# Optimization experiments

Hardware: AMD Instinct MI355X
Metric: run time of the kernel (lower is better)

## Reference

```python
import jax, jax.numpy as jnp
import numpy as np

NL = 192
SCALE = 1.5
SH_C0 = 0.28209479177387814
SH_C1 = 0.4886025119029199
SH_C2 = [1.0925484305920792, -1.0925484305920792, 0.31539156525252005, -1.0925484305920792, 0.5462742152960396]


def sh_eval(k, d):
    # k: (N, 3, 9) SH coeffs, d: (N, 3) directions -> (N, 3) rgb
    x, y, z = d[..., 0:1], d[..., 1:2], d[..., 2:3]
    return (SH_C0 * k[..., 0]
            - SH_C1 * y * k[..., 1]
            + SH_C1 * z * k[..., 2]
            - SH_C1 * x * k[..., 3]
            + SH_C2[0] * x * y * k[..., 4]
            + SH_C2[1] * y * z * k[..., 5]
            + SH_C2[2] * (2.0 * z * z - x * x - y * y) * k[..., 6]
            + SH_C2[3] * x * z * k[..., 7]
            + SH_C2[4] * (x * x - y * y) * k[..., 8])


def setup_inputs() -> dict:
    key = jax.random.key(0)
    k1, k2 = jax.random.split(key)
    N = 1048576
    x = jax.random.normal(k1, (N, 3), dtype=jnp.float32)
    d = jax.random.normal(k2, (N, 3), dtype=jnp.float32)
    voxel = jnp.ones((NL, NL, NL, 28), dtype=jnp.float32) / 100.0
    return {"x": x, "d": d, "voxel": voxel}


def reference(x, d, voxel):
    xs = x / SCALE
    mask = jnp.all(jnp.abs(xs) < 0.5, axis=1)  # (N,)
    # continuous grid coordinates, clipped like the original
    idx = jnp.clip(xs / (2.0 / NL) + NL / 2.0, 0.0, NL - 1.0)  # (N,3)
    xf = jnp.floor(idx)
    xc = jnp.ceil(idx)
    f = xf.astype(jnp.int32)
    c = xc.astype(jnp.int32)
    # 8 vertices in the ORIGINAL module's ordering (incl. its patch-layout quirk)
    vx = jnp.stack([f[:, 0], c[:, 0], f[:, 0], f[:, 0], f[:, 0], c[:, 0], c[:, 0], c[:, 0]], axis=1)
    vy = jnp.stack([f[:, 1], f[:, 1], c[:, 1], f[:, 1], c[:, 1], f[:, 1], c[:, 1], c[:, 1]], axis=1)
    vz = jnp.stack([f[:, 2], f[:, 2], f[:, 2], c[:, 2], c[:, 2], c[:, 2], f[:, 2], c[:, 2]], axis=1)
    v = voxel[vx, vy, vz]  # (N, 8, 28) gather
    # grid_sample trilinear weights on the 2x2x2 patch: slot j=(dd,hh,ww),
    # w-frac = t0, h-frac = t1, d-frac = t2 (align_corners=False, size 2 => frac = t)
    t = idx - xf  # (N,3)
    t0, t1, t2 = t[:, 0], t[:, 1], t[:, 2]
    u0, u1, u2 = 1.0 - t0, 1.0 - t1, 1.0 - t2
    w = jnp.stack([u2 * u1 * u0, u2 * u1 * t0, u2 * t1 * u0, u2 * t1 * t0,
                   t2 * u1 * u0, t2 * u1 * t0, t2 * t1 * u0, t2 * t1 * t0], axis=1)  # (N,8)
    feat = jnp.einsum('nk,nkc->nc', w, v)  # (N,28)
    sigma = jnp.where(mask, jax.nn.relu(feat[:, 0]), 0.0)  # (N,)
    k = feat[:, 1:].reshape(-1, 3, 9)
    color = jnp.where(mask[:, None], sh_eval(k, d), 0.0)  # (N,3)
    return color, sigma
```

## Files before the change

### kernel.cpp

```cpp
#include <hip/hip_runtime.h>


#define VNL 192

#define SH_C0f 0.28209479177387814f
#define SH_C1f 0.4886025119029199f
#define C2_0f  1.0925484305920792f
#define C2_1f (-1.0925484305920792f)
#define C2_2f  0.31539156525252005f
#define C2_3f (-1.0925484305920792f)
#define C2_4f  0.5462742152960396f

__global__ __launch_bounds__(256) void plen_fused_kernel(
    const float* __restrict__ x,
    const float* __restrict__ d,
    const float* __restrict__ voxel,
    float* __restrict__ out,
    int N)
{
    int i = blockIdx.x * 256 + threadIdx.x;
    const int lane = threadIdx.x & 63;
    const int g = lane >> 3;
    const int j = lane & 7;

    bool act = false;
    float px = 0.f, py = 0.f, pz = 0.f;
    float vdx = 0.f, vdy = 0.f, vdz = 0.f;
    if (i < N) {
        px = x[3 * i + 0] / 1.5f;
        py = x[3 * i + 1] / 1.5f;
        pz = x[3 * i + 2] / 1.5f;
        act = (fabsf(px) < 0.5f) && (fabsf(py) < 0.5f) && (fabsf(pz) < 0.5f);
        vdx = d[3 * i + 0];
        vdy = d[3 * i + 1];
        vdz = d[3 * i + 2];
        if (!act) {
            out[3 * i + 0] = 0.f;
            out[3 * i + 1] = 0.f;
            out[3 * i + 2] = 0.f;
            out[(size_t)3 * N + i] = 0.f;
        }
    }

    unsigned long long bal = __ballot(act);
    int nact = (int)__popcll(bal);

    for (int c = 0; c * 8 < nact; ++c) {
        int r = c * 8 + g;
        bool gact = (r < nact);
        int rr = gact ? r : 0;

        unsigned long long m = bal;
        for (int k = 0; k < rr; ++k) m &= (m - 1);
        int owner = (int)__builtin_ctzll(m);

        float ppx = __shfl(px,  owner);
        float ppy = __shfl(py,  owner);
        float ppz = __shfl(pz,  owner);
        float pdx = __shfl(vdx, owner);
        float pdy = __shfl(vdy, owner);
        float pdz = __shfl(vdz, owner);
        int   pi  = __shfl(i,   owner);

        if (gact) {
            const float step = 2.0f / (float)VNL;
            float ix = fminf(fmaxf(ppx / step + (float)(VNL / 2), 0.0f), (float)(VNL - 1));
            float iy = fminf(fmaxf(ppy / step + (float)(VNL / 2), 0.0f), (float)(VNL - 1));
            float iz = fminf(fmaxf(ppz / step + (float)(VNL / 2), 0.0f), (float)(VNL - 1));

            float fx = floorf(ix), fy = floorf(iy), fz = floorf(iz);
            int f0 = (int)fx, f1 = (int)fy, f2 = (int)fz;
            int c0i = (int)ceilf(ix), c1i = (int)ceilf(iy), c2i = (int)ceilf(iz);

            float t0 = ix - fx, t1 = iy - fy, t2 = iz - fz;
            float u0 = 1.0f - t0, u1 = 1.0f - t1, u2 = 1.0f - t2;

            float wj = ((j & 4) ? t2 : u2) * ((j & 2) ? t1 : u1) * ((j & 1) ? t0 : u0);

            int X = ((0xE2 >> j) & 1) ? c0i : f0;
            int Y = ((0xD4 >> j) & 1) ? c1i : f1;
            int Z = ((0xB8 >> j) & 1) ? c2i : f2;
            int off = ((X * VNL + Y) * VNL + Z) * 112;

            const char* cell = (const char*)voxel + (size_t)(unsigned)off;
            float4 v0 = *(const float4*)(cell +  0);
            float4 v1 = *(const float4*)(cell + 16);
            float4 v2 = *(const float4*)(cell + 32);
            float4 v3 = *(const float4*)(cell + 48);
            float4 v4 = *(const float4*)(cell + 64);
            float4 v5 = *(const float4*)(cell + 80);
            float4 v6 = *(const float4*)(cell + 96);

            float b1 = -SH_C1f * pdy;
            float b2 =  SH_C1f * pdz;
            float b3 = -SH_C1f * pdx;
            float b4 = C2_0f * pdx * pdy;
            float b5 = C2_1f * pdy * pdz;
            float b6 = C2_2f * (2.0f * pdz * pdz - pdx * pdx - pdy * pdy);
            float b7 = C2_3f * pdx * pdz;
            float b8 = C2_4f * (pdx * pdx - pdy * pdy);

            float cc0 = SH_C0f*v0.y + b1*v0.z + b2*v0.w + b3*v1.x + b4*v1.y
                      + b5*v1.z + b6*v1.w + b7*v2.x + b8*v2.y;
            float cc1 = SH_C0f*v2.z + b1*v2.w + b2*v3.x + b3*v3.y + b4*v3.z
                      + b5*v3.w + b6*v4.x + b7*v4.y + b8*v4.z;
            float cc2 = SH_C0f*v4.w + b1*v5.x + b2*v5.y + b3*v5.z + b4*v5.w
                      + b5*v6.x + b6*v6.y + b7*v6.z + b8*v6.w;
            cc0 *= wj; cc1 *= wj; cc2 *= wj;
            float ff0 = wj * v0.x;

            #pragma unroll
            for (int mm = 1; mm <= 4; mm <<= 1) {
                cc0 += __shfl_xor(cc0, mm);
                cc1 += __shfl_xor(cc1, mm);
                cc2 += __shfl_xor(cc2, mm);
                ff0 += __shfl_xor(ff0, mm);
            }

            if (j < 4) {
                float rv = (j == 0) ? cc0 : (j == 1) ? cc1 : (j == 2) ? cc2
                                                          : fmaxf(ff0, 0.0f);
                size_t a = (j < 3) ? ((size_t)3 * pi + j) : ((size_t)3 * N + pi);
                out[a] = rv;
            }
        }
    }
}

extern "C" void kernel_launch(void* const* d_in, const int* in_sizes, int n_in,
                              void* d_out, int out_size, void* d_ws, size_t ws_size,
                              hipStream_t stream) {
    const float* x     = (const float*)d_in[0];
    const float* d     = (const float*)d_in[1];
    const float* voxel = (const float*)d_in[2];
    float* out = (float*)d_out;
    int N = in_sizes[0] / 3;

    int grid = (N + 255) / 256;
    plen_fused_kernel<<<grid, 256, 0, stream>>>(x, d, voxel, out, N);
}
```

Before: 49.26 us.

## Compact active points across the block via LDS and use DPP reductions

New measurement: 47.65 us. 3.3% less time.

```diff
diff --git a/kernel.cpp b/kernel.cpp
--- a/kernel.cpp
+++ b/kernel.cpp
@@ -2,6 +2,8 @@
 
 
 #define VNL 192
+#define BLK 256
+#define WPB 4
 
 #define SH_C0f 0.28209479177387814f
 #define SH_C1f 0.4886025119029199f
@@ -11,15 +13,26 @@
 #define C2_3f (-1.0925484305920792f)
 #define C2_4f  0.5462742152960396f
 
-__global__ __launch_bounds__(256) void plen_fused_kernel(
+template <int CTRL>
+__device__ __forceinline__ float dpp_add(float v) {
+    int s = __builtin_amdgcn_update_dpp(0, __float_as_int(v), CTRL, 0xF, 0xF, true);
+    return v + __int_as_float(s);
+}
+
+__global__ __launch_bounds__(BLK) void plen_fused_kernel(
     const float* __restrict__ x,
     const float* __restrict__ d,
     const float* __restrict__ voxel,
     float* __restrict__ out,
     int N)
 {
-    int i = blockIdx.x * 256 + threadIdx.x;
-    const int lane = threadIdx.x & 63;
+    __shared__ __align__(16) float s_pool[BLK][8];
+    __shared__ unsigned s_wcnt[WPB];
+
+    const int tid  = threadIdx.x;
+    const int i    = blockIdx.x * BLK + tid;
+    const int wid  = tid >> 6;
+    const int lane = tid & 63;
     const int g = lane >> 3;
     const int j = lane & 7;
 
@@ -43,26 +56,37 @@
     }
 
     unsigned long long bal = __ballot(act);
-    int nact = (int)__popcll(bal);
+    unsigned wtot = (unsigned)__popcll(bal);
+    unsigned pre  = (unsigned)__popcll(bal & ((1ull << lane) - 1ull));
+    if (lane == 0) s_wcnt[wid] = wtot;
+    __syncthreads();
 
-    for (int c = 0; c * 8 < nact; ++c) {
-        int r = c * 8 + g;
-        bool gact = (r < nact);
-        int rr = gact ? r : 0;
+    unsigned n0 = s_wcnt[0], n1 = s_wcnt[1], n2 = s_wcnt[2], n3 = s_wcnt[3];
+    unsigned M = n0 + n1 + n2 + n3;
+    unsigned base = (wid > 0 ? n0 : 0u) + (wid > 1 ? n1 : 0u) + (wid > 2 ? n2 : 0u);
 
-        unsigned long long m = bal;
-        for (int k = 0; k < rr; ++k) m &= (m - 1);
-        int owner = (int)__builtin_ctzll(m);
+    if (act) {
+        unsigned slot = base + pre;
+        float4* rp = reinterpret_cast<float4*>(&s_pool[slot][0]);
+        rp[0] = make_float4(px, py, pz, __int_as_float(i));
+        rp[1] = make_float4(vdx, vdy, vdz, 0.f);
+    }
+    __syncthreads();
 
-        float ppx = __shfl(px,  owner);
-        float ppy = __shfl(py,  owner);
-        float ppz = __shfl(pz,  owner);
-        float pdx = __shfl(vdx, owner);
-        float pdy = __shfl(vdy, owner);
-        float pdz = __shfl(vdz, owner);
-        int   pi  = __shfl(i,   owner);
+    for (unsigned c = (unsigned)wid; c * 8u < M; c += WPB) {
+        unsigned r = c * 8u + (unsigned)g;
+        bool gact = (r < M);
+        unsigned rr = gact ? r : 0u;
+
+        const float4* rp = reinterpret_cast<const float4*>(&s_pool[rr][0]);
+        float4 e0 = rp[0];
+        float4 e1 = rp[1];
 
         if (gact) {
+            float ppx = e0.x, ppy = e0.y, ppz = e0.z;
+            int   pi  = __float_as_int(e0.w);
+            float pdx = e1.x, pdy = e1.y, pdz = e1.z;
+
             const float step = 2.0f / (float)VNL;
             float ix = fminf(fmaxf(ppx / step + (float)(VNL / 2), 0.0f), (float)(VNL - 1));
             float iy = fminf(fmaxf(ppy / step + (float)(VNL / 2), 0.0f), (float)(VNL - 1));
@@ -109,13 +133,12 @@
             cc0 *= wj; cc1 *= wj; cc2 *= wj;
             float ff0 = wj * v0.x;
 
-            #pragma unroll
-            for (int mm = 1; mm <= 4; mm <<= 1) {
-                cc0 += __shfl_xor(cc0, mm);
-                cc1 += __shfl_xor(cc1, mm);
-                cc2 += __shfl_xor(cc2, mm);
-                ff0 += __shfl_xor(ff0, mm);
-            }
+            cc0 = dpp_add<0xB1>(cc0); cc1 = dpp_add<0xB1>(cc1);
+            cc2 = dpp_add<0xB1>(cc2); ff0 = dpp_add<0xB1>(ff0);
+            cc0 = dpp_add<0x4E>(cc0); cc1 = dpp_add<0x4E>(cc1);
+            cc2 = dpp_add<0x4E>(cc2); ff0 = dpp_add<0x4E>(ff0);
+            cc0 = dpp_add<0x141>(cc0); cc1 = dpp_add<0x141>(cc1);
+            cc2 = dpp_add<0x141>(cc2); ff0 = dpp_add<0x141>(ff0);
 
             if (j < 4) {
                 float rv = (j == 0) ? cc0 : (j == 1) ? cc1 : (j == 2) ? cc2
@@ -136,6 +159,6 @@
     float* out = (float*)d_out;
     int N = in_sizes[0] / 3;
 
-    int grid = (N + 255) / 256;
-    plen_fused_kernel<<<grid, 256, 0, stream>>>(x, d, voxel, out, N);
+    int grid = (N + BLK - 1) / BLK;
+    plen_fused_kernel<<<grid, BLK, 0, stream>>>(x, d, voxel, out, N);
 }
```
